# Kernel tuning notes

Hardware: AMD Instinct MI355X
Metric: run time of the kernel (lower is better)

## Reference

```python
import jax, jax.numpy as jnp
import numpy as np

N = 100000      # number of entities
E = 400000      # number of edges (before self-loops)
D = 200         # feature_dim
D0 = 100        # init_fea_dim
NREL = 475      # 2*num_rels + 1 (self-loop relation = NREL-1)
NBR = 100       # num_base_r
B = 1024        # query batch
L = 2           # number of cells / layers
EPS = 1e-5


def _bn(x, g, b):
    # BatchNorm1d, training-mode batch statistics (biased var), per-feature affine
    m = jnp.mean(x, axis=0)
    v = jnp.var(x, axis=0)
    return (x - m) * jax.lax.rsqrt(v + EPS) * g + b


def setup_inputs() -> dict:
    key = jax.random.key(0)
    ks = jax.random.split(key, 12)
    return {
        # graph (edge list form of the DGL graph g)
        "src_id": jax.random.randint(ks[0], (E,), 0, N),
        "dst_id": jax.random.randint(ks[1], (E,), 0, N),
        "e_type": jax.random.randint(ks[2], (E,), 0, NREL - 1),  # NREL-1 reserved for self-loop
        # link-prediction queries
        "subj": jax.random.randint(ks[3], (B,), 0, N),
        "rel": jax.random.randint(ks[4], (B,), 0, NREL),
        # learned parameters
        "emb_h": jax.random.normal(ks[5], (N, D0), dtype=jnp.float32) * 0.02,
        "emb_e": jax.random.normal(ks[6], (NBR, D), dtype=jnp.float32) * 0.1,
        "lin_w": jax.random.normal(ks[7], (D0, D), dtype=jnp.float32) * (1.0 / np.sqrt(D0)),
        "lin_b": jnp.zeros((D,), dtype=jnp.float32),
        "rel_wt": jax.random.normal(ks[8], (NREL, NBR), dtype=jnp.float32) * 0.1,
        "w_rel": jax.random.normal(ks[9], (D, D), dtype=jnp.float32) * (1.0 / np.sqrt(D)),
        # per-cell params, stacked over L layers
        "agg_bn_g": jnp.ones((L, D), dtype=jnp.float32),
        "agg_bn_b": jnp.zeros((L, D), dtype=jnp.float32),
        "cell_bn_g": jnp.ones((L, D), dtype=jnp.float32),
        "cell_bn_b": jnp.zeros((L, D), dtype=jnp.float32),
        "concat_w": jax.random.normal(ks[10], (L, D, D), dtype=jnp.float32) * (1.0 / np.sqrt(D)),
        "concat_b": jnp.zeros((L, D), dtype=jnp.float32),
    }


def reference(src_id, dst_id, e_type, subj, rel,
              emb_h, emb_e, lin_w, lin_b, rel_wt, w_rel,
              agg_bn_g, agg_bn_b, cell_bn_g, cell_bn_b, concat_w, concat_b):
    nodes = jnp.arange(N, dtype=src_id.dtype)
    # append self-loops for every node, with the dedicated self-loop relation id
    src_f = jnp.concatenate([src_id, nodes])                      # [E+N]
    dst_f = jnp.concatenate([dst_id, nodes])                      # [E+N]
    et_f = jnp.concatenate([e_type, jnp.full((N,), NREL - 1, dtype=e_type.dtype)])

    all_ent = emb_h @ lin_w + lin_b                               # [N, D]
    rel_embed = rel_wt @ emb_e                                    # [NREL, D]

    for i in range(L):
        src_emb = all_ent[src_f]                                  # [E+N, D] per-edge gather
        hr = rel_embed[et_f]                                      # [E+N, D] per-edge gather
        zero_out = src_emb * hr                                   # pre_mult op (no BN/ReLU)
        agg = jax.ops.segment_sum(zero_out, dst_f, num_segments=N)  # edge -> node aggregation
        agg = jax.nn.relu(_bn(agg, agg_bn_g[i], agg_bn_b[i]))     # OpModule BN + ReLU
        h = agg @ concat_w[i] + concat_b[i]                       # Cell concat Linear (1 concat node)
        all_ent = jax.nn.relu(_bn(h, cell_bn_g[i], cell_bn_b[i]))  # Cell BN + ReLU
        rel_embed = rel_embed @ w_rel                             # per-layer relation transform

    # DistMult score function: [B, N]
    score = (all_ent[subj] * rel_embed[rel]) @ all_ent.T
    return score
```

## Files before the change

### kernel.cpp

```cpp
#include <hip/hip_runtime.h>


#define N_ENT  100000
#define N_EDGE 400000
#define D_     200
#define D0_    100
#define NREL_  475
#define B_     1024
#define GSTAT2 2048
#define KP_D   224
#define KP_D0  128

typedef unsigned short ushort_t;
typedef __attribute__((ext_vector_type(8))) short bf16x8;
typedef __attribute__((ext_vector_type(4))) float f32x4;

__device__ __forceinline__ ushort_t f2bf(float x) {
  unsigned u = __float_as_uint(x);
  return (ushort_t)((u + 0x7FFFu + ((u >> 16) & 1u)) >> 16);
}
__device__ __forceinline__ float bf2f(ushort_t h) {
  return __uint_as_float(((unsigned)h) << 16);
}

__device__ __forceinline__ void gld16(const void* g, void* l) {
  __builtin_amdgcn_global_load_lds(
      (const __attribute__((address_space(1))) unsigned*)g,
      (__attribute__((address_space(3))) unsigned*)l, 16, 0, 0);
}


__global__ void k_hist(const int* __restrict__ dst_id, int* __restrict__ cnt) {
  int e = blockIdx.x * 256 + threadIdx.x;
  if (e < N_EDGE) atomicAdd(&cnt[dst_id[e]], 1);
}

__global__ __launch_bounds__(256) void k_scan_block(const int* __restrict__ cnt,
                                                    int* __restrict__ rp,
                                                    int* __restrict__ bsum) {
  __shared__ int sm[256];
  int tid = threadIdx.x;
  int base = blockIdx.x * 1024 + tid * 4;
  int v0 = (base + 0 < N_ENT) ? cnt[base + 0] : 0;
  int v1 = (base + 1 < N_ENT) ? cnt[base + 1] : 0;
  int v2 = (base + 2 < N_ENT) ? cnt[base + 2] : 0;
  int v3 = (base + 3 < N_ENT) ? cnt[base + 3] : 0;
  int tsum = v0 + v1 + v2 + v3;
  sm[tid] = tsum;
  __syncthreads();
  for (int off = 1; off < 256; off <<= 1) {
    int t = (tid >= off) ? sm[tid - off] : 0;
    __syncthreads();
    sm[tid] += t;
    __syncthreads();
  }
  int run = sm[tid] - tsum;
  if (base + 0 < N_ENT) { rp[base + 0] = run; } run += v0;
  if (base + 1 < N_ENT) { rp[base + 1] = run; } run += v1;
  if (base + 2 < N_ENT) { rp[base + 2] = run; } run += v2;
  if (base + 3 < N_ENT) { rp[base + 3] = run; }
  if (tid == 255) bsum[blockIdx.x] = sm[255];
}

__global__ void k_scan_tops(int* __restrict__ bsum, int nb) {
  __shared__ int sm[256];
  int tid = threadIdx.x;
  int v = (tid < nb) ? bsum[tid] : 0;
  sm[tid] = v;
  __syncthreads();
  for (int off = 1; off < 256; off <<= 1) {
    int t = (tid >= off) ? sm[tid - off] : 0;
    __syncthreads();
    sm[tid] += t;
    __syncthreads();
  }
  if (tid < nb) bsum[tid] = sm[tid] - v;
}

__global__ void k_scan_add(int* __restrict__ rp, const int* __restrict__ bsum,
                           int* __restrict__ cursor) {
  int i = blockIdx.x * 256 + threadIdx.x;
  if (i < N_ENT) {
    int r = rp[i] + bsum[i >> 10];
    rp[i] = r;
    cursor[i] = r;
  }
}

__global__ void k_fill(const int* __restrict__ src_id, const int* __restrict__ dst_id,
                       const int* __restrict__ e_type, int* __restrict__ cursor,
                       int* __restrict__ cs, int* __restrict__ ct) {
  int e = blockIdx.x * 256 + threadIdx.x;
  if (e < N_EDGE) {
    int pos = atomicAdd(&cursor[dst_id[e]], 1);
    cs[pos] = src_id[e];
    ct[pos] = e_type[e];
  }
}


template <bool BN>
__global__ __launch_bounds__(256) void k_aggregate(const float* __restrict__ ent,
                                                   const float* __restrict__ relE,
                                                   const int* __restrict__ rp,
                                                   const int* __restrict__ cnt,
                                                   const int* __restrict__ cs,
                                                   const int* __restrict__ ct,
                                                   float* __restrict__ out,
                                                   const float* __restrict__ scale,
                                                   const float* __restrict__ shift) {
  const int wv = threadIdx.x >> 6;
  const int lane = threadIdx.x & 63;
  const int n = blockIdx.x * 4 + wv;
  if (n >= N_ENT || lane >= 50) return;
  const int f4 = lane * 4;

  float sc[4] = {0, 0, 0, 0}, sh[4] = {0, 0, 0, 0};
  if (BN) {
    float4 s4 = *(const float4*)(scale + f4);
    float4 h4 = *(const float4*)(shift + f4);
    sc[0] = s4.x; sc[1] = s4.y; sc[2] = s4.z; sc[3] = s4.w;
    sh[0] = h4.x; sh[1] = h4.y; sh[2] = h4.z; sh[3] = h4.w;
  }

  float ax[4], ay[4] = {0, 0, 0, 0}, az[4] = {0, 0, 0, 0}, aw[4] = {0, 0, 0, 0};
  {
    float4 e = *(const float4*)(ent + (long)n * D_ + f4);
    float4 r = *(const float4*)(relE + (long)(NREL_ - 1) * D_ + f4);
    float ee[4] = {e.x, e.y, e.z, e.w};
    float rr[4] = {r.x, r.y, r.z, r.w};
#pragma unroll
    for (int u = 0; u < 4; ++u) {
      if (BN) ee[u] = fmaxf(fmaf(ee[u], sc[u], sh[u]), 0.f);
      ax[u] = ee[u] * rr[u];
    }
  }

  int s0 = rp[n], e0 = s0 + cnt[n];
  int idx = s0;
  for (; idx + 4 <= e0; idx += 4) {
    int sA = cs[idx + 0], tA = ct[idx + 0];
    int sB = cs[idx + 1], tB = ct[idx + 1];
    int sC = cs[idx + 2], tC = ct[idx + 2];
    int sD = cs[idx + 3], tD = ct[idx + 3];
    float4 eA = *(const float4*)(ent + (long)sA * D_ + f4);
    float4 eB = *(const float4*)(ent + (long)sB * D_ + f4);
    float4 eC = *(const float4*)(ent + (long)sC * D_ + f4);
    float4 eD = *(const float4*)(ent + (long)sD * D_ + f4);
    float4 rA = *(const float4*)(relE + (long)tA * D_ + f4);
    float4 rB = *(const float4*)(relE + (long)tB * D_ + f4);
    float4 rC = *(const float4*)(relE + (long)tC * D_ + f4);
    float4 rD = *(const float4*)(relE + (long)tD * D_ + f4);
    float ea[4] = {eA.x, eA.y, eA.z, eA.w}, ra[4] = {rA.x, rA.y, rA.z, rA.w};
    float eb[4] = {eB.x, eB.y, eB.z, eB.w}, rb[4] = {rB.x, rB.y, rB.z, rB.w};
    float ec[4] = {eC.x, eC.y, eC.z, eC.w}, rc[4] = {rC.x, rC.y, rC.z, rC.w};
    float ed[4] = {eD.x, eD.y, eD.z, eD.w}, rd[4] = {rD.x, rD.y, rD.z, rD.w};
#pragma unroll
    for (int u = 0; u < 4; ++u) {
      if (BN) {
        ea[u] = fmaxf(fmaf(ea[u], sc[u], sh[u]), 0.f);
        eb[u] = fmaxf(fmaf(eb[u], sc[u], sh[u]), 0.f);
        ec[u] = fmaxf(fmaf(ec[u], sc[u], sh[u]), 0.f);
        ed[u] = fmaxf(fmaf(ed[u], sc[u], sh[u]), 0.f);
      }
      ax[u] = fmaf(ea[u], ra[u], ax[u]);
      ay[u] = fmaf(eb[u], rb[u], ay[u]);
      az[u] = fmaf(ec[u], rc[u], az[u]);
      aw[u] = fmaf(ed[u], rd[u], aw[u]);
    }
  }
  for (; idx < e0; ++idx) {
    int sA = cs[idx], tA = ct[idx];
    float4 eA = *(const float4*)(ent + (long)sA * D_ + f4);
    float4 rA = *(const float4*)(relE + (long)tA * D_ + f4);
    float ea[4] = {eA.x, eA.y, eA.z, eA.w}, ra[4] = {rA.x, rA.y, rA.z, rA.w};
#pragma unroll
    for (int u = 0; u < 4; ++u) {
      if (BN) ea[u] = fmaxf(fmaf(ea[u], sc[u], sh[u]), 0.f);
      ax[u] = fmaf(ea[u], ra[u], ax[u]);
    }
  }
  float4 o = make_float4((ax[0] + ay[0]) + (az[0] + aw[0]),
                         (ax[1] + ay[1]) + (az[1] + aw[1]),
                         (ax[2] + ay[2]) + (az[2] + aw[2]),
                         (ax[3] + ay[3]) + (az[3] + aw[3]));
  *(float4*)(out + (long)n * D_ + f4) = o;
}

__global__ __launch_bounds__(64) void k_colstats(const float* __restrict__ X,
                                                 double* __restrict__ part) {
  int t = threadIdx.x;
  if (t >= 50) return;
  double s0 = 0, s1 = 0, s2 = 0, s3 = 0, q0 = 0, q1 = 0, q2 = 0, q3 = 0;
  for (int r = blockIdx.x; r < N_ENT; r += GSTAT2) {
    float4 v = *(const float4*)(X + (long)r * D_ + t * 4);
    s0 += v.x; q0 += (double)v.x * v.x;
    s1 += v.y; q1 += (double)v.y * v.y;
    s2 += v.z; q2 += (double)v.z * v.z;
    s3 += v.w; q3 += (double)v.w * v.w;
  }
  long o = (long)blockIdx.x * 400 + t * 4;
  part[o + 0] = s0; part[o + 1] = s1; part[o + 2] = s2; part[o + 3] = s3;
  part[o + 200] = q0; part[o + 201] = q1; part[o + 202] = q2; part[o + 203] = q3;
}

__global__ __launch_bounds__(256) void k_bn_fin(const double* __restrict__ part,
                                                const float* __restrict__ g,
                                                const float* __restrict__ b,
                                                float* __restrict__ scale,
                                                float* __restrict__ shift) {
  int f = blockIdx.x;
  int tid = threadIdx.x;
  double S = 0.0, S2 = 0.0;
  for (int i = tid; i < GSTAT2; i += 256) {
    S += part[(long)i * 400 + f];
    S2 += part[(long)i * 400 + 200 + f];
  }
  __shared__ double smS[256], smS2[256];
  smS[tid] = S; smS2[tid] = S2;
  __syncthreads();
  for (int off = 128; off > 0; off >>= 1) {
    if (tid < off) { smS[tid] += smS[tid + off]; smS2[tid] += smS2[tid + off]; }
    __syncthreads();
  }
  if (tid == 0) {
    double mean = smS[0] / N_ENT;
    double var = smS2[0] / N_ENT - mean * mean;
    double inv = 1.0 / sqrt(var + 1e-5);
    float sc = g[f] * (float)inv;
    scale[f] = sc;
    shift[f] = b[f] - (float)mean * sc;
  }
}

__global__ __launch_bounds__(256) void k_bn_fin2(const double* __restrict__ pstat,
                                                 int nblk,
                                                 const float* __restrict__ g,
                                                 const float* __restrict__ b,
                                                 float* __restrict__ scale,
                                                 float* __restrict__ shift) {
  int f = blockIdx.x;
  int by = f >> 7, col = f & 127;
  int tid = threadIdx.x;
  double S = 0.0, S2 = 0.0;
  for (int bx = tid; bx < nblk; bx += 256) {
    long pb = (((long)bx * 2 + by) * 128 + col) * 2;
    S += pstat[pb];
    S2 += pstat[pb + 1];
  }
  __shared__ double smS[256], smS2[256];
  smS[tid] = S; smS2[tid] = S2;
  __syncthreads();
  for (int off = 128; off > 0; off >>= 1) {
    if (tid < off) { smS[tid] += smS[tid + off]; smS2[tid] += smS2[tid + off]; }
    __syncthreads();
  }
  if (tid == 0) {
    double mean = smS[0] / N_ENT;
    double var = smS2[0] / N_ENT - mean * mean;
    double inv = 1.0 / sqrt(var + 1e-5);
    float sc = g[f] * (float)inv;
    scale[f] = sc;
    shift[f] = b[f] - (float)mean * sc;
  }
}


#define NS_BLK 2048
#define Q_BLK  ((B_ * KP_D + 255) / 256)
__global__ void k_split_all(const float* __restrict__ X,
                            const float* __restrict__ scale,
                            const float* __restrict__ shift,
                            const float* __restrict__ relE,
                            const int* __restrict__ subj,
                            const int* __restrict__ rel,
                            ushort_t* __restrict__ H, ushort_t* __restrict__ L,
                            ushort_t* __restrict__ QH, ushort_t* __restrict__ QL) {
  if (blockIdx.x < NS_BLK) {
    const long total = (long)N_ENT * (KP_D / 4);
    for (long i4 = (long)blockIdx.x * 256 + threadIdx.x; i4 < total;
         i4 += (long)NS_BLK * 256) {
      int r = (int)(i4 / (KP_D / 4));
      int c4 = (int)(i4 % (KP_D / 4)) * 4;
      float vv[4] = {0.f, 0.f, 0.f, 0.f};
      if (c4 < D_) {
        float4 v = *(const float4*)(X + (long)r * D_ + c4);
        vv[0] = fmaxf(fmaf(v.x, scale[c4 + 0], shift[c4 + 0]), 0.f);
        vv[1] = fmaxf(fmaf(v.y, scale[c4 + 1], shift[c4 + 1]), 0.f);
        vv[2] = fmaxf(fmaf(v.z, scale[c4 + 2], shift[c4 + 2]), 0.f);
        vv[3] = fmaxf(fmaf(v.w, scale[c4 + 3], shift[c4 + 3]), 0.f);
      }
      ushort_t h[4], l[4];
#pragma unroll
      for (int t = 0; t < 4; t++) {
        h[t] = f2bf(vv[t]);
        l[t] = f2bf(vv[t] - bf2f(h[t]));
      }
      long o = (long)r * KP_D + c4;
      *(uint2*)(H + o) = make_uint2((unsigned)h[0] | ((unsigned)h[1] << 16),
                                    (unsigned)h[2] | ((unsigned)h[3] << 16));
      *(uint2*)(L + o) = make_uint2((unsigned)l[0] | ((unsigned)l[1] << 16),
                                    (unsigned)l[2] | ((unsigned)l[3] << 16));
    }
  } else {
    int i = (blockIdx.x - NS_BLK) * 256 + threadIdx.x;
    if (i >= B_ * KP_D) return;
    int b = i / KP_D, kp = i - b * KP_D;
    float v = 0.f;
    if (kp < D_) {
      float e = X[(long)subj[b] * D_ + kp];
      e = fmaxf(fmaf(e, scale[kp], shift[kp]), 0.f);
      v = e * relE[(long)rel[b] * D_ + kp];
    }
    ushort_t h = f2bf(v);
    QH[i] = h;
    QL[i] = f2bf(v - bf2f(h));
  }
}

__device__ __forceinline__ void tsplit_one(const float* __restrict__ W, int K,
                                           int Nc, int Kp, ushort_t* __restrict__ H,
                                           ushort_t* __restrict__ L, int i) {
  if (i >= Nc * Kp) return;
  int n = i / Kp, kp = i - n * Kp;
  float v = (kp < K) ? W[(long)kp * Nc + n] : 0.f;
  ushort_t h = f2bf(v);
  H[i] = h;
  L[i] = f2bf(v - bf2f(h));
}

__global__ void k_prep(const float* __restrict__ lin_w,
                       const float* __restrict__ concat_w,
                       const float* __restrict__ emb_e,
                       const float* __restrict__ w_rel,
                       ushort_t* __restrict__ linw_h, ushort_t* __restrict__ linw_l,
                       ushort_t* __restrict__ cw0_h, ushort_t* __restrict__ cw0_l,
                       ushort_t* __restrict__ cw1_h, ushort_t* __restrict__ cw1_l,
                       float* __restrict__ embeT, float* __restrict__ wrT) {
  int blk = blockIdx.x;
  int tid = threadIdx.x;
  if (blk < 100) {
    tsplit_one(lin_w, D0_, D_, KP_D0, linw_h, linw_l, blk * 256 + tid);
  } else if (blk < 275) {
    tsplit_one(concat_w, D_, D_, KP_D, cw0_h, cw0_l, (blk - 100) * 256 + tid);
  } else if (blk < 450) {
    tsplit_one(concat_w + D_ * D_, D_, D_, KP_D, cw1_h, cw1_l, (blk - 275) * 256 + tid);
  } else if (blk < 529) {
    int i = (blk - 450) * 256 + tid;
    if (i < D0_ * D_) { int r = i / D_, c = i - r * D_; embeT[c * D0_ + r] = emb_e[i]; }
  } else {
    int i = (blk - 529) * 256 + tid;
    if (i < D_ * D_) { int r = i / D_, c = i - r * D_; wrT[c * D_ + r] = w_rel[i]; }
  }
}

__global__ __launch_bounds__(256, 2) void k_score4(
    const ushort_t* __restrict__ Ah, const ushort_t* __restrict__ Al,
    const ushort_t* __restrict__ Bh, const ushort_t* __restrict__ Bl,
    float* __restrict__ C) {
  constexpr int KP = KP_D;
  __shared__ __align__(16) ushort_t lds[2 * 14336];
  const int tid = threadIdx.x;
  const int wave = tid >> 6, lane = tid & 63;
  const int l15 = lane & 15, l4 = lane >> 4;

  int g = (blockIdx.x & 7) * 1563 + (blockIdx.x >> 3);
  const int bm = (g & 7) * 128;
  const int bn = (g >> 3) * 64;

  bf16x8 qh[2][7], ql[2][7];
#pragma unroll
  for (int i = 0; i < 2; ++i) {
    long rowa = (long)(bm + wave * 32 + i * 16 + l15) * KP + l4 * 8;
#pragma unroll
    for (int k = 0; k < 7; ++k) {
      qh[i][k] = *(const bf16x8*)(Ah + rowa + k * 32);
      ql[i][k] = *(const bf16x8*)(Al + rowa + k * 32);
    }
  }

#pragma unroll
  for (int jj = 0; jj < 14; ++jj) {
    int c = wave * 14 + jj;
    int u = c * 64 + lane;
    int isl = (u >= 1792) ? 1 : 0;
    int u2 = u - isl * 1792;
    int kst = u2 >> 8;
    int rem = u2 & 255;
    int r = rem >> 2;
    int slot = rem & 3;
    int srcslot = slot ^ ((r >> 1) & 3);
    int rowg = bn + r; if (rowg > N_ENT - 1) rowg = N_ENT - 1;
    const ushort_t* src = (isl ? Bl : Bh) + (long)rowg * KP + kst * 32 + srcslot * 8;
    gld16(src, lds + c * 512);
  }
  __syncthreads();

  f32x4 acc[2][4] = {};
#pragma unroll
  for (int k = 0; k < 7; ++k) {
    bf16x8 eh[4], el[4];
#pragma unroll
    for (int j = 0; j < 4; ++j) {
      int rB = j * 16 + l15;
      int slot = l4 ^ ((rB >> 1) & 3);
      int ad = k * 2048 + rB * 32 + slot * 8;
      eh[j] = *(const bf16x8*)(lds + ad);
      el[j] = *(const bf16x8*)(lds + 14336 + ad);
    }
    __builtin_amdgcn_s_setprio(1);
#pragma unroll
    for (int i = 0; i < 2; ++i)
#pragma unroll
      for (int j = 0; j < 4; ++j) {
        acc[i][j] = __builtin_amdgcn_mfma_f32_16x16x32_bf16(eh[j], qh[i][k], acc[i][j], 0, 0, 0);
        acc[i][j] = __builtin_amdgcn_mfma_f32_16x16x32_bf16(eh[j], ql[i][k], acc[i][j], 0, 0, 0);
        acc[i][j] = __builtin_amdgcn_mfma_f32_16x16x32_bf16(el[j], qh[i][k], acc[i][j], 0, 0, 0);
      }
    __builtin_amdgcn_s_setprio(0);
  }

#pragma unroll
  for (int i = 0; i < 2; ++i) {
    int m = bm + wave * 32 + i * 16 + l15;
#pragma unroll
    for (int j = 0; j < 4; ++j) {
      int nb = bn + j * 16 + l4 * 4;
      if (nb < N_ENT) {
        float4 o = make_float4(acc[i][j][0], acc[i][j][1], acc[i][j][2], acc[i][j][3]);
        *(float4*)(C + (long)m * N_ENT + nb) = o;
      }
    }
  }
}

template <bool BN_A, bool HAS_BIAS, bool STATS>
__global__ __launch_bounds__(256, 2) void k_mfma_af32(
    const float* __restrict__ A, int lda, int K,
    const ushort_t* __restrict__ Bh, const ushort_t* __restrict__ Bl,
    float* __restrict__ C, int M, int Nc, int Kp, long ldc,
    const float* __restrict__ scale, const float* __restrict__ shift,
    const float* __restrict__ bias, double* __restrict__ pstat) {
  __shared__ __align__(16) ushort_t lds[2 * 16384];
  __shared__ float sc_lds[KP_D], sh_lds[KP_D];
  const int tid = threadIdx.x;
  const int wave = tid >> 6, lane = tid & 63;
  const int bm = blockIdx.x * 128, bn = blockIdx.y * 128;
  const int wr = (wave >> 1) * 64, wc = (wave & 1) * 64;
  const int l15 = lane & 15, l4 = lane >> 4;
  const int NT = Kp >> 5;

  if (BN_A) {
    for (int i = tid; i < Kp; i += 256) {
      sc_lds[i] = (i < K) ? scale[i] : 0.f;
      sh_lds[i] = (i < K) ? shift[i] : 0.f;
    }
    __syncthreads();
  }

  const int ar = tid >> 1;
  const int acb = (tid & 1) * 16;
  int arow = bm + ar; if (arow > M - 1) arow = M - 1;
  const int aswz = (ar >> 1) & 3;
  const int s0 = (((acb >> 3) + 0) ^ aswz) * 8;
  const int s1 = (((acb >> 3) + 1) ^ aswz) * 8;

  auto loadA = [&](int kt, float4* va) {
    int kc = kt * 32 + acb;
    const float* ap = A + (long)arow * lda + kc;
    if (kc + 16 <= K) {
#pragma unroll
      for (int q = 0; q < 4; q++) va[q] = *(const float4*)(ap + q * 4);
    } else {
#pragma unroll
      for (int q = 0; q < 4; q++) {
        float t0 = (kc + q * 4 + 0 < K) ? ap[q * 4 + 0] : 0.f;
        float t1 = (kc + q * 4 + 1 < K) ? ap[q * 4 + 1] : 0.f;
        float t2 = (kc + q * 4 + 2 < K) ? ap[q * 4 + 2] : 0.f;
        float t3 = (kc + q * 4 + 3 < K) ? ap[q * 4 + 3] : 0.f;
        va[q] = make_float4(t0, t1, t2, t3);
      }
    }
  };

  auto writeA = [&](int kt, int ph, float4* va) {
    float v[16];
#pragma unroll
    for (int q = 0; q < 4; q++) {
      v[q * 4 + 0] = va[q].x; v[q * 4 + 1] = va[q].y;
      v[q * 4 + 2] = va[q].z; v[q * 4 + 3] = va[q].w;
    }
    if (BN_A) {
      int kc = kt * 32 + acb;
#pragma unroll
      for (int e = 0; e < 16; e++) {
        int col = kc + e;
        if (col < K) v[e] = fmaxf(fmaf(v[e], sc_lds[col], sh_lds[col]), 0.f);
      }
    }
    unsigned hh[8], ll[8];
#pragma unroll
    for (int e = 0; e < 8; e++) {
      ushort_t h0 = f2bf(v[2 * e]), h1 = f2bf(v[2 * e + 1]);
      ushort_t l0 = f2bf(v[2 * e] - bf2f(h0)), l1 = f2bf(v[2 * e + 1] - bf2f(h1));
      hh[e] = (unsigned)h0 | ((unsigned)h1 << 16);
      ll[e] = (unsigned)l0 | ((unsigned)l1 << 16);
    }
    ushort_t* baseA = lds + ph * 16384 + ar * 32;
    *(uint4*)(baseA + s0) = make_uint4(hh[0], hh[1], hh[2], hh[3]);
    *(uint4*)(baseA + s1) = make_uint4(hh[4], hh[5], hh[6], hh[7]);
    ushort_t* baseL = baseA + 4096;
    *(uint4*)(baseL + s0) = make_uint4(ll[0], ll[1], ll[2], ll[3]);
    *(uint4*)(baseL + s1) = make_uint4(ll[4], ll[5], ll[6], ll[7]);
  };

  auto stageB = [&](int kt, int ph) {
#pragma unroll
    for (int j = 0; j < 4; ++j) {
      int c = 16 + wave * 4 + j;
      int buf = c >> 3;
      int r = (c & 7) * 16 + (lane >> 2);
      int sg = (lane & 3) ^ ((r >> 1) & 3);
      const ushort_t* bp = (buf == 2) ? Bh : Bl;
      int rowg = bn + r; if (rowg > Nc - 1) rowg = Nc - 1;
      gld16(bp + (long)rowg * Kp + kt * 32 + sg * 8, lds + ph * 16384 + c * 512);
    }
  };

  f32x4 acc[4][4] = {};
  {
    float4 va[4];
    loadA(0, va);
    writeA(0, 0, va);
    stageB(0, 0);
  }
  __syncthreads();
  int p = 0;
  for (int t = 0; t < NT; ++t) {
    float4 va[4];
    const bool pre = (t + 1 < NT);
    if (pre) {
      loadA(t + 1, va);
      stageB(t + 1, p ^ 1);
    }
    const ushort_t* base = lds + p * 16384;
    bf16x8 a_h[4], a_l[4], b_h[4], b_l[4];
#pragma unroll
    for (int i = 0; i < 4; i++) {
      int rA = wr + i * 16 + l15;
      int sA = (l4 ^ ((rA >> 1) & 3)) * 8;
      a_h[i] = *(const bf16x8*)(base + rA * 32 + sA);
      a_l[i] = *(const bf16x8*)(base + 4096 + rA * 32 + sA);
      int rB = wc + i * 16 + l15;
      int sB = (l4 ^ ((rB >> 1) & 3)) * 8;
      b_h[i] = *(const bf16x8*)(base + 8192 + rB * 32 + sB);
      b_l[i] = *(const bf16x8*)(base + 12288 + rB * 32 + sB);
    }
#pragma unroll
    for (int i = 0; i < 4; i++)
#pragma unroll
      for (int j = 0; j < 4; j++) {
        acc[i][j] = __builtin_amdgcn_mfma_f32_16x16x32_bf16(a_h[i], b_h[j], acc[i][j], 0, 0, 0);
        acc[i][j] = __builtin_amdgcn_mfma_f32_16x16x32_bf16(a_l[i], b_h[j], acc[i][j], 0, 0, 0);
        acc[i][j] = __builtin_amdgcn_mfma_f32_16x16x32_bf16(a_h[i], b_l[j], acc[i][j], 0, 0, 0);
      }
    if (pre) writeA(t + 1, p ^ 1, va);
    __syncthreads();
    p ^= 1;
  }

#pragma unroll
  for (int i = 0; i < 4; i++) {
    int mrow = bm + wr + i * 16 + l4 * 4;
#pragma unroll
    for (int j = 0; j < 4; j++) {
      int n = bn + wc + j * 16 + l15;
      if (n >= Nc) continue;
      float bb = HAS_BIAS ? bias[n] : 0.f;
#pragma unroll
      for (int v = 0; v < 4; v++) {
        int m = mrow + v;
        if (m < M) C[(long)m * ldc + n] = acc[i][j][v] + bb;
      }
    }
  }

  if (STATS) {
    double* sred = (double*)lds;
    double* qred = ((double*)lds) + 1024;
    const int slot = (wave >> 1) * 4 + l4;
#pragma unroll
    for (int j = 0; j < 4; j++) {
      int colt = wc + j * 16 + l15;
      int n = bn + colt;
      double s = 0.0, q = 0.0;
      if (n < Nc) {
        float bb = HAS_BIAS ? bias[n] : 0.f;
#pragma unroll
        for (int i = 0; i < 4; i++) {
          int mrow = bm + wr + i * 16 + l4 * 4;
#pragma unroll
          for (int v = 0; v < 4; v++) {
            if (mrow + v < M) {
              float val = acc[i][j][v] + bb;
              s += val;
              q += (double)val * val;
            }
          }
        }
      }
      sred[slot * 128 + colt] = s;
      qred[slot * 128 + colt] = q;
    }
    __syncthreads();
    if (tid < 128) {
      double S = 0.0, Q = 0.0;
#pragma unroll
      for (int sl = 0; sl < 8; sl++) {
        S += sred[sl * 128 + tid];
        Q += qred[sl * 128 + tid];
      }
      long pb = (((long)blockIdx.x * 2 + blockIdx.y) * 128 + tid) * 2;
      pstat[pb] = S;
      pstat[pb + 1] = Q;
    }
  }
}

template <int TM, int TN>
__global__ __launch_bounds__(256) void k_gemm_abt(
    const float* __restrict__ A, const float* __restrict__ Bm, float* __restrict__ C,
    int M, int Nc, int K, long ldc) {
  constexpr int BM = TM * 16, BN = TN * 16, KC = 20;
  __shared__ float As[BM * KC];
  __shared__ float Bs[BN * KC];
  const int tid = threadIdx.x;
  const int tx = tid & 15, ty = tid >> 4;
  const int bm = blockIdx.x * BM, bn = blockIdx.y * BN;
  float acc[TM][TN];
#pragma unroll
  for (int i = 0; i < TM; i++)
#pragma unroll
    for (int j = 0; j < TN; j++) acc[i][j] = 0.f;
  for (int kc = 0; kc < K; kc += KC) {
    for (int i4 = tid; i4 < BM * 5; i4 += 256) {
      int r = i4 / 5, kq = (i4 - r * 5) * 4;
      int row = bm + r; if (row > M - 1) row = M - 1;
      *(float4*)(As + r * KC + kq) = *(const float4*)(A + (long)row * K + kc + kq);
    }
    for (int i4 = tid; i4 < BN * 5; i4 += 256) {
      int r = i4 / 5, kq = (i4 - r * 5) * 4;
      int row = bn + r; if (row > Nc - 1) row = Nc - 1;
      *(float4*)(Bs + r * KC + kq) = *(const float4*)(Bm + (long)row * K + kc + kq);
    }
    __syncthreads();
#pragma unroll
    for (int k4 = 0; k4 < KC; k4 += 4) {
      float4 af[TM], bf[TN];
#pragma unroll
      for (int i = 0; i < TM; i++) af[i] = *(const float4*)(As + (i * 16 + ty) * KC + k4);
#pragma unroll
      for (int j = 0; j < TN; j++) bf[j] = *(const float4*)(Bs + (j * 16 + tx) * KC + k4);
#pragma unroll
      for (int i = 0; i < TM; i++)
#pragma unroll
        for (int j = 0; j < TN; j++) {
          acc[i][j] = fmaf(af[i].x, bf[j].x, acc[i][j]);
          acc[i][j] = fmaf(af[i].y, bf[j].y, acc[i][j]);
          acc[i][j] = fmaf(af[i].z, bf[j].z, acc[i][j]);
          acc[i][j] = fmaf(af[i].w, bf[j].w, acc[i][j]);
        }
    }
    __syncthreads();
  }
#pragma unroll
  for (int i = 0; i < TM; i++) {
    int m = bm + i * 16 + ty;
    if (m >= M) continue;
#pragma unroll
    for (int j = 0; j < TN; j++) {
      int n = bn + j * 16 + tx;
      if (n < Nc) C[(long)m * ldc + n] = acc[i][j];
    }
  }
}


extern "C" void kernel_launch(void* const* d_in, const int* in_sizes, int n_in,
                              void* d_out, int out_size, void* d_ws, size_t ws_size,
                              hipStream_t stream) {
  const int* src_id = (const int*)d_in[0];
  const int* dst_id = (const int*)d_in[1];
  const int* e_type = (const int*)d_in[2];
  const int* subj = (const int*)d_in[3];
  const int* rel = (const int*)d_in[4];
  const float* emb_h = (const float*)d_in[5];
  const float* emb_e = (const float*)d_in[6];
  const float* lin_w = (const float*)d_in[7];
  const float* lin_b = (const float*)d_in[8];
  const float* rel_wt = (const float*)d_in[9];
  const float* w_rel = (const float*)d_in[10];
  const float* agg_bn_g = (const float*)d_in[11];
  const float* agg_bn_b = (const float*)d_in[12];
  const float* cell_bn_g = (const float*)d_in[13];
  const float* cell_bn_b = (const float*)d_in[14];
  const float* concat_w = (const float*)d_in[15];
  const float* concat_b = (const float*)d_in[16];
  float* out = (float*)d_out;

  char* w = (char*)d_ws;
  ushort_t* ent_h = (ushort_t*)(w + 0);
  ushort_t* ent_l = (ushort_t*)(w + 44800000);
  ushort_t* q_h   = (ushort_t*)(w + 89600000);
  ushort_t* q_l   = (ushort_t*)(w + 90112000);

  char* ob = (char*)d_out;
  float* ent    = (float*)(ob + 0);
  float* tmp    = (float*)(ob + 80000000);
  double* part  = (double*)(ob + 160000000);
  int* counts   = (int*)(ob + 166600000);
  int* row_ptr  = (int*)(ob + 167000000);
  int* cursor   = (int*)(ob + 167400000);
  int* csr_src  = (int*)(ob + 167800000);
  int* csr_et   = (int*)(ob + 169400000);
  float* relA   = (float*)(ob + 171800000);
  float* relB   = (float*)(ob + 172180000);
  float* embeT  = (float*)(ob + 172560000);
  float* wrT    = (float*)(ob + 172640000);
  ushort_t* linw_h = (ushort_t*)(ob + 172800000);
  ushort_t* linw_l = (ushort_t*)(ob + 172851200);
  ushort_t* cw0_h  = (ushort_t*)(ob + 172902400);
  ushort_t* cw0_l  = (ushort_t*)(ob + 172992000);
  ushort_t* cw1_h  = (ushort_t*)(ob + 173081600);
  ushort_t* cw1_l  = (ushort_t*)(ob + 173171200);
  float* scaleb = (float*)(ob + 173260800);
  float* shiftb = (float*)(ob + 173261824);
  int* bsum     = (int*)(ob + 173262848);
  double* pstat = (double*)(ob + 173263360);

  (void)hipMemsetAsync(counts, 0, N_ENT * sizeof(int), stream);
  k_hist<<<(N_EDGE + 255) / 256, 256, 0, stream>>>(dst_id, counts);
  const int NB = (N_ENT + 1023) / 1024;
  k_scan_block<<<NB, 256, 0, stream>>>(counts, row_ptr, bsum);
  k_scan_tops<<<1, 256, 0, stream>>>(bsum, NB);
  k_scan_add<<<(N_ENT + 255) / 256, 256, 0, stream>>>(row_ptr, bsum, cursor);
  k_fill<<<(N_EDGE + 255) / 256, 256, 0, stream>>>(src_id, dst_id, e_type, cursor,
                                                   csr_src, csr_et);

  k_prep<<<686, 256, 0, stream>>>(lin_w, concat_w, emb_e, w_rel,
                                  linw_h, linw_l, cw0_h, cw0_l, cw1_h, cw1_l,
                                  embeT, wrT);

  const int GM = (N_ENT + 127) / 128;
  const int GA = (N_ENT + 3) / 4;

  k_mfma_af32<false, true, false><<<dim3(GM, 2), 256, 0, stream>>>(
      emb_h, D0_, D0_, linw_h, linw_l, ent, N_ENT, D_, KP_D0, (long)D_,
      nullptr, nullptr, lin_b, nullptr);
  k_gemm_abt<8, 4><<<dim3(4, 4), 256, 0, stream>>>(rel_wt, embeT, relA, NREL_, D_,
                                                   D0_, (long)D_);

  k_aggregate<false><<<GA, 256, 0, stream>>>(ent, relA, row_ptr, counts,
                                             csr_src, csr_et, tmp, nullptr, nullptr);
  k_colstats<<<GSTAT2, 64, 0, stream>>>(tmp, part);
  k_bn_fin<<<D_, 256, 0, stream>>>(part, agg_bn_g, agg_bn_b, scaleb, shiftb);
  k_mfma_af32<true, true, true><<<dim3(GM, 2), 256, 0, stream>>>(
      tmp, D_, D_, cw0_h, cw0_l, ent, N_ENT, D_, KP_D, (long)D_,
      scaleb, shiftb, concat_b, pstat);
  k_bn_fin2<<<D_, 256, 0, stream>>>(pstat, GM, cell_bn_g, cell_bn_b, scaleb, shiftb);
  k_gemm_abt<8, 4><<<dim3(4, 4), 256, 0, stream>>>(relA, wrT, relB, NREL_, D_, D_,
                                                   (long)D_);

  k_aggregate<true><<<GA, 256, 0, stream>>>(ent, relB, row_ptr, counts,
                                            csr_src, csr_et, tmp, scaleb, shiftb);
  k_colstats<<<GSTAT2, 64, 0, stream>>>(tmp, part);
  k_bn_fin<<<D_, 256, 0, stream>>>(part, agg_bn_g + D_, agg_bn_b + D_, scaleb, shiftb);
  k_mfma_af32<true, true, true><<<dim3(GM, 2), 256, 0, stream>>>(
      tmp, D_, D_, cw1_h, cw1_l, ent, N_ENT, D_, KP_D, (long)D_,
      scaleb, shiftb, concat_b + D_, pstat);
  k_bn_fin2<<<D_, 256, 0, stream>>>(pstat, GM, cell_bn_g + D_, cell_bn_b + D_,
                                    scaleb, shiftb);
  k_gemm_abt<8, 4><<<dim3(4, 4), 256, 0, stream>>>(relB, wrT, relA, NREL_, D_, D_,
                                                   (long)D_);
  k_split_all<<<NS_BLK + Q_BLK, 256, 0, stream>>>(ent, scaleb, shiftb, relA,
                                                  subj, rel, ent_h, ent_l, q_h, q_l);

  k_score4<<<dim3(8 * 1563), 256, 0, stream>>>(q_h, q_l, ent_h, ent_l, out);
}
```

Before: 966.9 us.

## Fuse BN column statistics into edge aggregation kernel

The aggregation kernel now processes 16 nodes per wave (64 per block) and accumulates per-feature sum and sum-of-squares in double, reducing them across waves in shared memory and writing per-block partials. This removes the separate column-statistics pass that re-read the whole N x D aggregate from memory. The cost is fewer, longer-lived blocks with serialized per-node work per wave, which may lower latency hiding for the irregular gathers, plus double-precision accumulation inside the gather loop.

```diff
diff --git a/kernel.cpp b/kernel.cpp
--- a/kernel.cpp
+++ b/kernel.cpp
@@ -7,7 +7,6 @@
 #define D0_    100
 #define NREL_  475
 #define B_     1024
-#define GSTAT2 2048
 #define KP_D   224
 #define KP_D0  128
 
@@ -108,103 +107,115 @@
                                                    const int* __restrict__ ct,
                                                    float* __restrict__ out,
                                                    const float* __restrict__ scale,
-                                                   const float* __restrict__ shift) {
+                                                   const float* __restrict__ shift,
+                                                   double* __restrict__ pstat) {
+  __shared__ double sred[4 * 200];
+  __shared__ double qred[4 * 200];
   const int wv = threadIdx.x >> 6;
   const int lane = threadIdx.x & 63;
-  const int n = blockIdx.x * 4 + wv;
-  if (n >= N_ENT || lane >= 50) return;
   const int f4 = lane * 4;
-
-  float sc[4] = {0, 0, 0, 0}, sh[4] = {0, 0, 0, 0};
-  if (BN) {
-    float4 s4 = *(const float4*)(scale + f4);
-    float4 h4 = *(const float4*)(shift + f4);
-    sc[0] = s4.x; sc[1] = s4.y; sc[2] = s4.z; sc[3] = s4.w;
-    sh[0] = h4.x; sh[1] = h4.y; sh[2] = h4.z; sh[3] = h4.w;
-  }
-
-  float ax[4], ay[4] = {0, 0, 0, 0}, az[4] = {0, 0, 0, 0}, aw[4] = {0, 0, 0, 0};
-  {
-    float4 e = *(const float4*)(ent + (long)n * D_ + f4);
-    float4 r = *(const float4*)(relE + (long)(NREL_ - 1) * D_ + f4);
-    float ee[4] = {e.x, e.y, e.z, e.w};
-    float rr[4] = {r.x, r.y, r.z, r.w};
+  double sa[4] = {0, 0, 0, 0}, qa[4] = {0, 0, 0, 0};
+
+  if (lane < 50) {
+    float sc[4] = {0, 0, 0, 0}, sh[4] = {0, 0, 0, 0};
+    if (BN) {
+      float4 s4 = *(const float4*)(scale + f4);
+      float4 h4 = *(const float4*)(shift + f4);
+      sc[0] = s4.x; sc[1] = s4.y; sc[2] = s4.z; sc[3] = s4.w;
+      sh[0] = h4.x; sh[1] = h4.y; sh[2] = h4.z; sh[3] = h4.w;
+    }
+    float4 rself = *(const float4*)(relE + (long)(NREL_ - 1) * D_ + f4);
+    float rs[4] = {rself.x, rself.y, rself.z, rself.w};
+
+    for (int t = 0; t < 16; ++t) {
+      int n = blockIdx.x * 64 + wv * 16 + t;
+      if (n >= N_ENT) break;
+
+      float ax[4], ay[4] = {0, 0, 0, 0}, az[4] = {0, 0, 0, 0}, aw[4] = {0, 0, 0, 0};
+      {
+        float4 e = *(const float4*)(ent + (long)n * D_ + f4);
+        float ee[4] = {e.x, e.y, e.z, e.w};
+#pragma unroll
+        for (int u = 0; u < 4; ++u) {
+          if (BN) ee[u] = fmaxf(fmaf(ee[u], sc[u], sh[u]), 0.f);
+          ax[u] = ee[u] * rs[u];
+        }
+      }
+
+      int s0 = rp[n], e0 = s0 + cnt[n];
+      int idx = s0;
+      for (; idx + 4 <= e0; idx += 4) {
+        int sA = cs[idx + 0], tA = ct[idx + 0];
+        int sB = cs[idx + 1], tB = ct[idx + 1];
+        int sC = cs[idx + 2], tC = ct[idx + 2];
+        int sD = cs[idx + 3], tD = ct[idx + 3];
+        float4 eA = *(const float4*)(ent + (long)sA * D_ + f4);
+        float4 eB = *(const float4*)(ent + (long)sB * D_ + f4);
+        float4 eC = *(const float4*)(ent + (long)sC * D_ + f4);
+        float4 eD = *(const float4*)(ent + (long)sD * D_ + f4);
+        float4 rA = *(const float4*)(relE + (long)tA * D_ + f4);
+        float4 rB = *(const float4*)(relE + (long)tB * D_ + f4);
+        float4 rC = *(const float4*)(relE + (long)tC * D_ + f4);
+        float4 rD = *(const float4*)(relE + (long)tD * D_ + f4);
+        float ea[4] = {eA.x, eA.y, eA.z, eA.w}, ra[4] = {rA.x, rA.y, rA.z, rA.w};
+        float eb[4] = {eB.x, eB.y, eB.z, eB.w}, rb[4] = {rB.x, rB.y, rB.z, rB.w};
+        float ec[4] = {eC.x, eC.y, eC.z, eC.w}, rc[4] = {rC.x, rC.y, rC.z, rC.w};
+        float ed[4] = {eD.x, eD.y, eD.z, eD.w}, rd[4] = {rD.x, rD.y, rD.z, rD.w};
+#pragma unroll
+        for (int u = 0; u < 4; ++u) {
+          if (BN) {
+            ea[u] = fmaxf(fmaf(ea[u], sc[u], sh[u]), 0.f);
+            eb[u] = fmaxf(fmaf(eb[u], sc[u], sh[u]), 0.f);
+            ec[u] = fmaxf(fmaf(ec[u], sc[u], sh[u]), 0.f);
+            ed[u] = fmaxf(fmaf(ed[u], sc[u], sh[u]), 0.f);
+          }
+          ax[u] = fmaf(ea[u], ra[u], ax[u]);
+          ay[u] = fmaf(eb[u], rb[u], ay[u]);
+          az[u] = fmaf(ec[u], rc[u], az[u]);
+          aw[u] = fmaf(ed[u], rd[u], aw[u]);
+        }
+      }
+      for (; idx < e0; ++idx) {
+        int sA = cs[idx], tA = ct[idx];
+        float4 eA = *(const float4*)(ent + (long)sA * D_ + f4);
+        float4 rA = *(const float4*)(relE + (long)tA * D_ + f4);
+        float ea[4] = {eA.x, eA.y, eA.z, eA.w}, ra[4] = {rA.x, rA.y, rA.z, rA.w};
+#pragma unroll
+        for (int u = 0; u < 4; ++u) {
+          if (BN) ea[u] = fmaxf(fmaf(ea[u], sc[u], sh[u]), 0.f);
+          ax[u] = fmaf(ea[u], ra[u], ax[u]);
+        }
+      }
+      float o[4];
+#pragma unroll
+      for (int u = 0; u < 4; ++u) {
+        o[u] = (ax[u] + ay[u]) + (az[u] + aw[u]);
+        sa[u] += o[u];
+        qa[u] += (double)o[u] * o[u];
+      }
+      *(float4*)(out + (long)n * D_ + f4) = make_float4(o[0], o[1], o[2], o[3]);
+    }
+  }
+
+  if (lane < 50) {
 #pragma unroll
     for (int u = 0; u < 4; ++u) {
-      if (BN) ee[u] = fmaxf(fmaf(ee[u], sc[u], sh[u]), 0.f);
-      ax[u] = ee[u] * rr[u];
-    }
-  }
-
-  int s0 = rp[n], e0 = s0 + cnt[n];
-  int idx = s0;
-  for (; idx + 4 <= e0; idx += 4) {
-    int sA = cs[idx + 0], tA = ct[idx + 0];
-    int sB = cs[idx + 1], tB = ct[idx + 1];
-    int sC = cs[idx + 2], tC = ct[idx + 2];
-    int sD = cs[idx + 3], tD = ct[idx + 3];
-    float4 eA = *(const float4*)(ent + (long)sA * D_ + f4);
-    float4 eB = *(const float4*)(ent + (long)sB * D_ + f4);
-    float4 eC = *(const float4*)(ent + (long)sC * D_ + f4);
-    float4 eD = *(const float4*)(ent + (long)sD * D_ + f4);
-    float4 rA = *(const float4*)(relE + (long)tA * D_ + f4);
-    float4 rB = *(const float4*)(relE + (long)tB * D_ + f4);
-    float4 rC = *(const float4*)(relE + (long)tC * D_ + f4);
-    float4 rD = *(const float4*)(relE + (long)tD * D_ + f4);
-    float ea[4] = {eA.x, eA.y, eA.z, eA.w}, ra[4] = {rA.x, rA.y, rA.z, rA.w};
-    float eb[4] = {eB.x, eB.y, eB.z, eB.w}, rb[4] = {rB.x, rB.y, rB.z, rB.w};
-    float ec[4] = {eC.x, eC.y, eC.z, eC.w}, rc[4] = {rC.x, rC.y, rC.z, rC.w};
-    float ed[4] = {eD.x, eD.y, eD.z, eD.w}, rd[4] = {rD.x, rD.y, rD.z, rD.w};
-#pragma unroll
-    for (int u = 0; u < 4; ++u) {
-      if (BN) {
-        ea[u] = fmaxf(fmaf(ea[u], sc[u], sh[u]), 0.f);
-        eb[u] = fmaxf(fmaf(eb[u], sc[u], sh[u]), 0.f);
-        ec[u] = fmaxf(fmaf(ec[u], sc[u], sh[u]), 0.f);
-        ed[u] = fmaxf(fmaf(ed[u], sc[u], sh[u]), 0.f);
-      }
-      ax[u] = fmaf(ea[u], ra[u], ax[u]);
-      ay[u] = fmaf(eb[u], rb[u], ay[u]);
-      az[u] = fmaf(ec[u], rc[u], az[u]);
-      aw[u] = fmaf(ed[u], rd[u], aw[u]);
-    }
-  }
-  for (; idx < e0; ++idx) {
-    int sA = cs[idx], tA = ct[idx];
-    float4 eA = *(const float4*)(ent + (long)sA * D_ + f4);
-    float4 rA = *(const float4*)(relE + (long)tA * D_ + f4);
-    float ea[4] = {eA.x, eA.y, eA.z, eA.w}, ra[4] = {rA.x, rA.y, rA.z, rA.w};
-#pragma unroll
-    for (int u = 0; u < 4; ++u) {
-      if (BN) ea[u] = fmaxf(fmaf(ea[u], sc[u], sh[u]), 0.f);
-      ax[u] = fmaf(ea[u], ra[u], ax[u]);
-    }
-  }
-  float4 o = make_float4((ax[0] + ay[0]) + (az[0] + aw[0]),
-                         (ax[1] + ay[1]) + (az[1] + aw[1]),
-                         (ax[2] + ay[2]) + (az[2] + aw[2]),
-                         (ax[3] + ay[3]) + (az[3] + aw[3]));
-  *(float4*)(out + (long)n * D_ + f4) = o;
-}
-
-__global__ __launch_bounds__(64) void k_colstats(const float* __restrict__ X,
-                                                 double* __restrict__ part) {
-  int t = threadIdx.x;
-  if (t >= 50) return;
-  double s0 = 0, s1 = 0, s2 = 0, s3 = 0, q0 = 0, q1 = 0, q2 = 0, q3 = 0;
-  for (int r = blockIdx.x; r < N_ENT; r += GSTAT2) {
-    float4 v = *(const float4*)(X + (long)r * D_ + t * 4);
-    s0 += v.x; q0 += (double)v.x * v.x;
-    s1 += v.y; q1 += (double)v.y * v.y;
-    s2 += v.z; q2 += (double)v.z * v.z;
-    s3 += v.w; q3 += (double)v.w * v.w;
-  }
-  long o = (long)blockIdx.x * 400 + t * 4;
-  part[o + 0] = s0; part[o + 1] = s1; part[o + 2] = s2; part[o + 3] = s3;
-  part[o + 200] = q0; part[o + 201] = q1; part[o + 202] = q2; part[o + 203] = q3;
+      sred[wv * 200 + f4 + u] = sa[u];
+      qred[wv * 200 + f4 + u] = qa[u];
+    }
+  }
+  __syncthreads();
+  int tid = threadIdx.x;
+  if (tid < 200) {
+    double S = (sred[tid] + sred[200 + tid]) + (sred[400 + tid] + sred[600 + tid]);
+    double Q = (qred[tid] + qred[200 + tid]) + (qred[400 + tid] + qred[600 + tid]);
+    pstat[(long)blockIdx.x * 400 + tid] = S;
+    pstat[(long)blockIdx.x * 400 + 200 + tid] = Q;
+  }
 }
 
 __global__ __launch_bounds__(256) void k_bn_fin(const double* __restrict__ part,
+                                                int nblk,
                                                 const float* __restrict__ g,
                                                 const float* __restrict__ b,
                                                 float* __restrict__ scale,
@@ -212,7 +223,7 @@
   int f = blockIdx.x;
   int tid = threadIdx.x;
   double S = 0.0, S2 = 0.0;
-  for (int i = tid; i < GSTAT2; i += 256) {
+  for (int i = tid; i < nblk; i += 256) {
     S += part[(long)i * 400 + f];
     S2 += part[(long)i * 400 + 200 + f];
   }
@@ -752,7 +763,7 @@
                                   embeT, wrT);
 
   const int GM = (N_ENT + 127) / 128;
-  const int GA = (N_ENT + 3) / 4;
+  const int GA = (N_ENT + 63) / 64;
 
   k_mfma_af32<false, true, false><<<dim3(GM, 2), 256, 0, stream>>>(
       emb_h, D0_, D0_, linw_h, linw_l, ent, N_ENT, D_, KP_D0, (long)D_,
@@ -761,9 +772,9 @@
                                                    D0_, (long)D_);
 
   k_aggregate<false><<<GA, 256, 0, stream>>>(ent, relA, row_ptr, counts,
-                                             csr_src, csr_et, tmp, nullptr, nullptr);
-  k_colstats<<<GSTAT2, 64, 0, stream>>>(tmp, part);
-  k_bn_fin<<<D_, 256, 0, stream>>>(part, agg_bn_g, agg_bn_b, scaleb, shiftb);
+                                             csr_src, csr_et, tmp, nullptr, nullptr,
+                                             part);
+  k_bn_fin<<<D_, 256, 0, stream>>>(part, GA, agg_bn_g, agg_bn_b, scaleb, shiftb);
   k_mfma_af32<true, true, true><<<dim3(GM, 2), 256, 0, stream>>>(
       tmp, D_, D_, cw0_h, cw0_l, ent, N_ENT, D_, KP_D, (long)D_,
       scaleb, shiftb, concat_b, pstat);
@@ -772,9 +783,10 @@
                                                    (long)D_);
 
   k_aggregate<true><<<GA, 256, 0, stream>>>(ent, relB, row_ptr, counts,
-                                            csr_src, csr_et, tmp, scaleb, shiftb);
-  k_colstats<<<GSTAT2, 64, 0, stream>>>(tmp, part);
-  k_bn_fin<<<D_, 256, 0, stream>>>(part, agg_bn_g + D_, agg_bn_b + D_, scaleb, shiftb);
+                                            csr_src, csr_et, tmp, scaleb, shiftb,
+                                            part);
+  k_bn_fin<<<D_, 256, 0, stream>>>(part, GA, agg_bn_g + D_, agg_bn_b + D_,
+                                   scaleb, shiftb);
   k_mfma_af32<true, true, true><<<dim3(GM, 2), 256, 0, stream>>>(
       tmp, D_, D_, cw1_h, cw1_l, ent, N_ENT, D_, KP_D, (long)D_,
       scaleb, shiftb, concat_b + D_, pstat);
```

Result: no change. 957.5 us, median of 2 (-1.0%).
